# Kernel tuning notes

Hardware: AMD Instinct MI355X
Metric: run time of the kernel (lower is better)

## Reference

```python
import jax, jax.numpy as jnp
import numpy as np

B, L, DIM, N, D = 8, 273, 1536, 12, 128
ZS, F_HIS = 256, 32  # image tokens per frame, cache_frame_max
EPS = 1e-6


def rmsnorm(x, g, eps=EPS):
    return x * jax.lax.rsqrt(jnp.mean(x * x, axis=-1, keepdims=True) + eps) * g


def rope_apply(x, freqs):
    # x: [B, T, N, D]; freqs: [T, D//2] angles. Rotate consecutive pairs.
    xp = x.reshape(*x.shape[:-1], D // 2, 2)
    c = jnp.cos(freqs)[None, :, None, :]
    s = jnp.sin(freqs)[None, :, None, :]
    o1 = xp[..., 0] * c - xp[..., 1] * s
    o2 = xp[..., 0] * s + xp[..., 1] * c
    return jnp.stack([o1, o2], axis=-1).reshape(x.shape)


def setup_inputs() -> dict:
    key = jax.random.key(0)
    ks = jax.random.split(key, 10)
    rn = lambda k, shp, sc=1.0: jax.random.normal(k, shp, dtype=jnp.float32) * sc
    return {
        "x": rn(ks[0], (B, L, DIM)),
        "w_q": rn(ks[1], (DIM, DIM), 0.02), "b_q": jnp.zeros((DIM,), jnp.float32),
        "w_k": rn(ks[2], (DIM, DIM), 0.02), "b_k": jnp.zeros((DIM,), jnp.float32),
        "w_v": rn(ks[3], (DIM, DIM), 0.02), "b_v": jnp.zeros((DIM,), jnp.float32),
        "w_o": rn(ks[4], (DIM, DIM), 0.02), "b_o": jnp.zeros((DIM,), jnp.float32),
        "g_q": jnp.ones((DIM,), jnp.float32), "g_k": jnp.ones((DIM,), jnp.float32),
        "cache_k": rn(ks[5], (B, F_HIS * L, N, D)),
        "cache_v": rn(ks[6], (B, F_HIS * L, N, D)),
        "rope_table": jax.random.uniform(ks[7], (64, L, D // 2), dtype=jnp.float32) * (2.0 * np.pi),
        "read_rope_indices": jnp.arange(F_HIS, dtype=jnp.int32),
        "current_frame_idx": 20,
    }


def reference(x, w_q, b_q, w_k, b_k, w_v, b_v, w_o, b_o, g_q, g_k,
              cache_k, cache_v, rope_table, read_rope_indices, current_frame_idx):
    b, s = x.shape[:2]
    f = 1  # one new frame per step (s == L)
    # qkv projections with RMSNorm over full dim (pre head split)
    q = rmsnorm(x @ w_q.T + b_q, g_q).reshape(b, s, N, D)
    k = rmsnorm(x @ w_k.T + b_k, g_k).reshape(b, s, N, D)
    v = (x @ w_v.T + b_v).reshape(b, s, N, D)
    # KV-cache ring-buffer store at slot = frame_idx % cache_frame_max
    slot = current_frame_idx % F_HIS
    cache_k = jax.lax.dynamic_update_slice(cache_k, k, (0, slot * L, 0, 0))
    cache_v = jax.lax.dynamic_update_slice(cache_v, v, (0, slot * L, 0, 0))
    # RoPE angles: history for each cache slot, last for the current frame
    freqs_his = rope_table[read_rope_indices].reshape(F_HIS * L, D // 2)
    freqs_last = rope_table[current_frame_idx]  # [L, D//2]
    q_r = rope_apply(q, freqs_last)
    k_r = rope_apply(cache_k, freqs_his)
    # frame-major views: [b, frames, tokens_per_frame, n, d]
    q_r = q_r.reshape(b, f, L, N, D)
    k_r = k_r.reshape(b, F_HIS, L, N, D)
    v_his = cache_v.reshape(b, F_HIS, L, N, D)
    q_img, k_img, v_img = q_r[:, :, :ZS], k_r[:, :, :ZS], v_his[:, :, :ZS]
    # temporal attention per spatial (image) token, non-causal, masked to valid frames
    scale = 1.0 / jnp.sqrt(jnp.asarray(D, jnp.float32))
    scores = jnp.einsum('bfznd,bgznd->bznfg', q_img, k_img) * scale  # [b,zs,n,f,f_his]
    valid = jnp.minimum(current_frame_idx + 1, F_HIS)
    keep = jnp.arange(F_HIS) < valid
    scores = jnp.where(keep[None, None, None, None, :], scores, -1e30)
    p = jax.nn.softmax(scores, axis=-1)
    x_img = jnp.einsum('bznfg,bgznd->bfznd', p, v_img)  # [b, f, zs, n, d]
    # condition tokens bypass attention: pass through v of the current frame
    v_cond = v.reshape(b, f, L, N, D)[:, :, ZS:]
    out = jnp.concatenate([x_img, v_cond], axis=2).reshape(b, s, N * D)
    return out @ w_o.T + b_o


if __name__ == '__main__':
    o = reference(**setup_inputs())
    print(o.shape)
```

## Files before the change

kernel.cpp:

```cpp
#include <hip/hip_runtime.h>
#include <hip/hip_bf16.h>
#include <stdint.h>

typedef unsigned short u16;
typedef __attribute__((ext_vector_type(8))) short bf16x8;
typedef __attribute__((ext_vector_type(4))) float f32x4;

#define B_    8
#define L_    273
#define DIM_  1536
#define NH_   12
#define DH_   128
#define ZS_   256
#define FH_   32
#define MROWS (B_ * L_)
#define MPAD  2304
#define NQKV  4608

#define OFF_XB    0ULL
#define OFF_WB    7077888ULL
#define OFF_WOB   21233664ULL
#define OFF_BQKV  25952256ULL
#define OFF_CQKV  25970688ULL
#define OFF_ATTN  47204352ULL
#define OFF_SC    54282240ULL

__device__ __forceinline__ u16 f2bf(float f) {
  __hip_bfloat16 h = __float2bfloat16(f);
  return *reinterpret_cast<u16*>(&h);
}
__device__ __forceinline__ float bf2f(u16 v) {
  uint32_t u = ((uint32_t)v) << 16;
  return __uint_as_float(u);
}

__device__ __forceinline__ void gload_lds16(const u16* g, u16* l) {
  __builtin_amdgcn_global_load_lds(
      (const __attribute__((address_space(1))) void*)g,
      (__attribute__((address_space(3))) void*)l,
      16, 0, 0);
}

__global__ void cast_pad8_kernel(const float* __restrict__ src, u16* __restrict__ dst,
                                 int n_src8, int n_tot8) {
  int i = blockIdx.x * 256 + threadIdx.x;
  if (i >= n_tot8) return;
  uint4 o;
  if (i < n_src8) {
    const float4 a = ((const float4*)src)[i * 2];
    const float4 b = ((const float4*)src)[i * 2 + 1];
    o.x = (uint32_t)f2bf(a.x) | ((uint32_t)f2bf(a.y) << 16);
    o.y = (uint32_t)f2bf(a.z) | ((uint32_t)f2bf(a.w) << 16);
    o.z = (uint32_t)f2bf(b.x) | ((uint32_t)f2bf(b.y) << 16);
    o.w = (uint32_t)f2bf(b.z) | ((uint32_t)f2bf(b.w) << 16);
  } else {
    o = make_uint4(0, 0, 0, 0);
  }
  ((uint4*)dst)[i] = o;
}

__global__ void pack_bias_kernel(const float* __restrict__ bq, const float* __restrict__ bk,
                                 const float* __restrict__ bv, float* __restrict__ dst) {
  int i = blockIdx.x * 256 + threadIdx.x;
  if (i >= NQKV) return;
  float v;
  if (i < DIM_)            v = bq[i];
  else if (i < 2 * DIM_)   v = bk[i - DIM_];
  else                     v = bv[i - 2 * DIM_];
  dst[i] = v;
}

__global__ __launch_bounds__(256)
void sincos_kernel(const float* __restrict__ rope_table, const int* __restrict__ rope_idx,
                   float* __restrict__ sctab) {
  const int idx = blockIdx.x * 4 + (threadIdx.x >> 6);
  const int j = threadIdx.x & 63;
  const int f = idx / ZS_, z = idx % ZS_;
  const int fi = rope_idx[f];
  const float fr = rope_table[((size_t)fi * L_ + z) * 64 + j];
  float sn, cn;
  __sincosf(fr, &sn, &cn);
  *(float2*)&sctab[((size_t)idx << 7) + 2 * j] = make_float2(sn, cn);
}

__global__ __launch_bounds__(256)
void gemm_bt_kernel(const u16* __restrict__ A, const u16* __restrict__ Bm,
                    const float* __restrict__ bias, void* __restrict__ Cv,
                    int K, int ldc, int Mvalid, int bf16out) {
  const int tn = blockIdx.x, tm = blockIdx.y;
  const int tid = threadIdx.x;
  const int lane = tid & 63;
  const int wid = tid >> 6;
  const int wm = wid >> 1, wn = wid & 1;

  __shared__ __align__(16) u16 As[128 * 32];
  __shared__ __align__(16) u16 Bs[128 * 32];

  f32x4 acc[4][4] = {};

  const int srow = tid >> 2;
  const int scol = (tid & 3) * 8;
  const u16* Abase = A + (size_t)(tm * 128 + srow) * K + scol;
  const u16* Bbase = Bm + (size_t)(tn * 128 + srow) * K + scol;
  u16* lAs = &As[srow * 32 + scol];
  u16* lBs = &Bs[srow * 32 + scol];
  const size_t rstep = (size_t)64 * K;

  const int ko = (lane >> 4) * 8;
  const int rA = wm * 64 + (lane & 15);
  const int rB = wn * 64 + (lane & 15);

  for (int kt = 0; kt < K; kt += 32) {
    __syncthreads();
    gload_lds16(Abase + kt,         lAs);
    gload_lds16(Abase + kt + rstep, lAs + 64 * 32);
    gload_lds16(Bbase + kt,         lBs);
    gload_lds16(Bbase + kt + rstep, lBs + 64 * 32);
    __syncthreads();

    bf16x8 af[4], bfr[4];
#pragma unroll
    for (int f = 0; f < 4; ++f) {
      af[f]  = *(const bf16x8*)&As[(rA + f * 16) * 32 + ko];
      bfr[f] = *(const bf16x8*)&Bs[(rB + f * 16) * 32 + ko];
    }
#pragma unroll
    for (int fm = 0; fm < 4; ++fm)
#pragma unroll
      for (int fn = 0; fn < 4; ++fn)
        acc[fm][fn] = __builtin_amdgcn_mfma_f32_16x16x32_bf16(af[fm], bfr[fn], acc[fm][fn], 0, 0, 0);
  }

  const int m0 = tm * 128 + wm * 64 + (lane >> 4) * 4;
  const int n0 = tn * 128 + wn * 64 + (lane & 15);
#pragma unroll
  for (int fm = 0; fm < 4; ++fm) {
#pragma unroll
    for (int fn = 0; fn < 4; ++fn) {
      const int n = n0 + fn * 16;
      const float bv = bias[n];
#pragma unroll
      for (int r = 0; r < 4; ++r) {
        const int m = m0 + fm * 16 + r;
        if (m < Mvalid) {
          const float val = acc[fm][fn][r] + bv;
          if (bf16out) ((u16*)Cv)[(size_t)m * ldc + n] = f2bf(val);
          else         ((float*)Cv)[(size_t)m * ldc + n] = val;
        }
      }
    }
  }
}

__global__ __launch_bounds__(256)
void rmsnorm_rope_kernel(u16* __restrict__ C, const float* __restrict__ g_q,
                         const float* __restrict__ g_k, const float* __restrict__ rope_table,
                         const int* __restrict__ cf_ptr) {
  const int z = blockIdx.x % ZS_;
  const int b = blockIdx.x / ZS_;
  const int m = b * L_ + z;
  const int tid = threadIdx.x;
  const int cf = *cf_ptr;
  u16* row = C + (size_t)m * NQKV;
  __shared__ float red[4];

  for (int sec = 0; sec < 2; ++sec) {
    u16* p = row + sec * DIM_;
    const float* gw = sec ? g_k : g_q;
    float vx[3], vy[3];
    float ss = 0.f;
#pragma unroll
    for (int j = 0; j < 3; ++j) {
      int pj = tid + j * 256;
      uint32_t u = *(const uint32_t*)&p[pj * 2];
      vx[j] = bf2f((u16)(u & 0xffff));
      vy[j] = bf2f((u16)(u >> 16));
      ss += vx[j] * vx[j] + vy[j] * vy[j];
    }
#pragma unroll
    for (int o = 32; o; o >>= 1) ss += __shfl_xor(ss, o);
    if ((tid & 63) == 0) red[tid >> 6] = ss;
    __syncthreads();
    const float tot = red[0] + red[1] + red[2] + red[3];
    const float r = rsqrtf(tot * (1.f / DIM_) + 1e-6f);
#pragma unroll
    for (int j = 0; j < 3; ++j) {
      int pj = tid + j * 256;
      float y0 = vx[j] * r * gw[pj * 2];
      float y1 = vy[j] * r * gw[pj * 2 + 1];
      if (sec == 0) {
        float fr = rope_table[((size_t)cf * L_ + z) * 64 + (pj & 63)];
        float sn, cn;
        __sincosf(fr, &sn, &cn);
        float o0 = y0 * cn - y1 * sn;
        float o1 = y0 * sn + y1 * cn;
        y0 = o0; y1 = o1;
      }
      *(uint32_t*)&p[pj * 2] = (uint32_t)f2bf(y0) | ((uint32_t)f2bf(y1) << 16);
    }
    __syncthreads();
  }
}

__global__ __launch_bounds__(256)
void attention_kernel(const u16* __restrict__ Cq, const float* __restrict__ cache_k,
                      const float* __restrict__ cache_v, const float* __restrict__ sctab,
                      const int* __restrict__ cf_ptr, u16* __restrict__ attn_in) {
  const int w = blockIdx.x * 4 + (threadIdx.x >> 6);
  const int lane = threadIdx.x & 63;
  const int hp = w % 6;
  const int z = (w / 6) % ZS_;
  const int b = w / (6 * ZS_);
  const int h = lane >> 5, il = lane & 31;
  const int n = hp * 2 + h;
  const int d0 = il * 4;
  const int cf = *cf_ptr;
  const int slot = cf % FH_;
  const int valid = min(cf + 1, FH_);

  const size_t crow = (size_t)(b * L_ + z) * NQKV + n * DH_ + d0;
  float q0, q1, q2, q3;
  {
    ushort4 qv = *(const ushort4*)&Cq[crow];
    q0 = bf2f(qv.x); q1 = bf2f(qv.y); q2 = bf2f(qv.z); q3 = bf2f(qv.w);
  }

  float mx = -1e30f, lsum = 0.f;
  float a0 = 0.f, a1 = 0.f, a2 = 0.f, a3 = 0.f;
  for (int g = 0; g < valid; ++g) {
    const float4 sc = *(const float4*)&sctab[((size_t)(g * ZS_ + z) << 7) + d0];
    float k0, k1, k2, k3, v0, v1, v2, v3;
    if (g == slot) {
      ushort4 kv = *(const ushort4*)&Cq[crow + DIM_];
      ushort4 vv = *(const ushort4*)&Cq[crow + 2 * DIM_];
      k0 = bf2f(kv.x); k1 = bf2f(kv.y); k2 = bf2f(kv.z); k3 = bf2f(kv.w);
      v0 = bf2f(vv.x); v1 = bf2f(vv.y); v2 = bf2f(vv.z); v3 = bf2f(vv.w);
    } else {
      const size_t coff = ((((size_t)b * FH_ + g) * L_ + z) * NH_ + n) * DH_ + d0;
      const float4 kk = *(const float4*)&cache_k[coff];
      const float4 vv = *(const float4*)&cache_v[coff];
      k0 = kk.x; k1 = kk.y; k2 = kk.z; k3 = kk.w;
      v0 = vv.x; v1 = vv.y; v2 = vv.z; v3 = vv.w;
    }
    const float kr0 = k0 * sc.y - k1 * sc.x;
    const float kr1 = k0 * sc.x + k1 * sc.y;
    const float kr2 = k2 * sc.w - k3 * sc.z;
    const float kr3 = k2 * sc.z + k3 * sc.w;
    float part = q0 * kr0 + q1 * kr1 + q2 * kr2 + q3 * kr3;
#pragma unroll
    for (int o = 16; o; o >>= 1) part += __shfl_xor(part, o);
    const float score = part * 0.088388347648318447f;
    const float nm = fmaxf(mx, score);
    const float scl = __expf(mx - nm);
    const float pw = __expf(score - nm);
    lsum = lsum * scl + pw;
    a0 = a0 * scl + pw * v0;
    a1 = a1 * scl + pw * v1;
    a2 = a2 * scl + pw * v2;
    a3 = a3 * scl + pw * v3;
    mx = nm;
  }
  const float inv = 1.f / lsum;
  uint2 o;
  o.x = (uint32_t)f2bf(a0 * inv) | ((uint32_t)f2bf(a1 * inv) << 16);
  o.y = (uint32_t)f2bf(a2 * inv) | ((uint32_t)f2bf(a3 * inv) << 16);
  *(uint2*)&attn_in[(size_t)(b * L_ + z) * DIM_ + n * DH_ + d0] = o;
}

__global__ void vcond_kernel(const u16* __restrict__ Cq, u16* __restrict__ attn_in) {
  int i = blockIdx.x * 256 + threadIdx.x;
  const int tot = B_ * (L_ - ZS_) * DIM_ / 8;
  if (i >= tot) return;
  int e = i * 8;
  int col = e % DIM_;
  int r = e / DIM_;
  int b = r / (L_ - ZS_);
  int lz = r % (L_ - ZS_);
  size_t mrow = (size_t)b * L_ + ZS_ + lz;
  *(uint4*)&attn_in[mrow * DIM_ + col] = *(const uint4*)&Cq[mrow * NQKV + 2 * DIM_ + col];
}

extern "C" void kernel_launch(void* const* d_in, const int* in_sizes, int n_in,
                              void* d_out, int out_size, void* d_ws, size_t ws_size,
                              hipStream_t stream) {
  const float* x       = (const float*)d_in[0];
  const float* w_q     = (const float*)d_in[1];
  const float* b_q     = (const float*)d_in[2];
  const float* w_k     = (const float*)d_in[3];
  const float* b_k     = (const float*)d_in[4];
  const float* w_v     = (const float*)d_in[5];
  const float* b_v     = (const float*)d_in[6];
  const float* w_o     = (const float*)d_in[7];
  const float* b_o     = (const float*)d_in[8];
  const float* g_q     = (const float*)d_in[9];
  const float* g_k     = (const float*)d_in[10];
  const float* cache_k = (const float*)d_in[11];
  const float* cache_v = (const float*)d_in[12];
  const float* rope_tb = (const float*)d_in[13];
  const int*   rope_ix = (const int*)d_in[14];
  const int*   cf      = (const int*)d_in[15];

  char* ws = (char*)d_ws;
  u16*   xb      = (u16*)(ws + OFF_XB);
  u16*   wb      = (u16*)(ws + OFF_WB);
  u16*   wob     = (u16*)(ws + OFF_WOB);
  float* bqkv    = (float*)(ws + OFF_BQKV);
  u16*   Cq      = (u16*)(ws + OFF_CQKV);
  u16*   attn_in = (u16*)(ws + OFF_ATTN);
  float* sctab   = (float*)(ws + OFF_SC);

  const int WN = DIM_ * DIM_;
  const int WN8 = WN / 8;
  const int X8 = MROWS * DIM_ / 8;
  const int XT8 = MPAD * DIM_ / 8;

  cast_pad8_kernel<<<(XT8 + 255) / 256, 256, 0, stream>>>(x, xb, X8, XT8);
  cast_pad8_kernel<<<(WN8 + 255) / 256, 256, 0, stream>>>(w_q, wb,          WN8, WN8);
  cast_pad8_kernel<<<(WN8 + 255) / 256, 256, 0, stream>>>(w_k, wb + WN,     WN8, WN8);
  cast_pad8_kernel<<<(WN8 + 255) / 256, 256, 0, stream>>>(w_v, wb + 2 * WN, WN8, WN8);
  cast_pad8_kernel<<<(WN8 + 255) / 256, 256, 0, stream>>>(w_o, wob,         WN8, WN8);
  pack_bias_kernel<<<(NQKV + 255) / 256, 256, 0, stream>>>(b_q, b_k, b_v, bqkv);
  sincos_kernel<<<FH_ * ZS_ / 4, 256, 0, stream>>>(rope_tb, rope_ix, sctab);

  gemm_bt_kernel<<<dim3(NQKV / 128, MPAD / 128), 256, 0, stream>>>(xb, wb, bqkv, Cq, DIM_, NQKV, MPAD, 1);

  rmsnorm_rope_kernel<<<B_ * ZS_, 256, 0, stream>>>(Cq, g_q, g_k, rope_tb, cf);

  attention_kernel<<<(B_ * ZS_ * 6) / 4, 256, 0, stream>>>(Cq, cache_k, cache_v, sctab, cf, attn_in);

  vcond_kernel<<<(B_ * (L_ - ZS_) * DIM_ / 8 + 255) / 256, 256, 0, stream>>>(Cq, attn_in);

  gemm_bt_kernel<<<dim3(DIM_ / 128, MPAD / 128), 256, 0, stream>>>(attn_in, wob, b_o, (float*)d_out, DIM_, DIM_, MROWS, 0);
}
```

Baseline: 250.1 us.

## Fuse prep kernels, double-buffer GEMM, split-K output projection, split attention frames

Merges the five casts, bias packing and sincos table into one prep kernel, and folds the v_cond copy into the attention launch to cut launch count. The GEMM gains double-buffered LDS so global loads overlap MFMA work. The output projection is split-K into two partial buffers (reusing workspace regions) with a separate reduce kernel adding bias. Attention splits each item's frame loop across two waves and merges them with an online-softmax combine through LDS. Split-K adds extra fp32 traffic and a reduce pass, and the partial buffers overlap earlier workspace regions.

```diff
diff --git a/kernel.cpp b/kernel.cpp
--- a/kernel.cpp
+++ b/kernel.cpp
@@ -16,6 +16,26 @@
 #define MROWS (B_ * L_)
 #define MPAD  2304
 #define NQKV  4608
+#define WN_   (DIM_ * DIM_)
+#define WN8_  (WN_ / 8)
+#define X8_   (MROWS * DIM_ / 8)
+#define XT8_  (MPAD * DIM_ / 8)
+
+#define N0_ 442368
+#define N1_ 737280
+#define N2_ 1032192
+#define N3_ 1327104
+#define N4_ 1622016
+#define N5_ 1626624
+#define N6_ 2150912
+#define PREP_BLKS 8402
+
+#define ATTN_ITEMS (B_ * ZS_ * 6)
+#define ATTN_BLKS  (ATTN_ITEMS / 2)
+#define VCOND_TOT  (B_ * (L_ - ZS_) * DIM_ / 8)
+#define VCOND_BLKS ((VCOND_TOT + 255) / 256)
+
+#define KSPLIT 768
 
 #define OFF_XB    0ULL
 #define OFF_WB    7077888ULL
@@ -24,6 +44,8 @@
 #define OFF_CQKV  25970688ULL
 #define OFF_ATTN  47204352ULL
 #define OFF_SC    54282240ULL
+#define OFF_P0    0ULL
+#define OFF_P1    25970688ULL
 
 __device__ __forceinline__ u16 f2bf(float f) {
   __hip_bfloat16 h = __float2bfloat16(f);
@@ -41,14 +63,12 @@
       16, 0, 0);
 }
 
-__global__ void cast_pad8_kernel(const float* __restrict__ src, u16* __restrict__ dst,
-                                 int n_src8, int n_tot8) {
-  int i = blockIdx.x * 256 + threadIdx.x;
-  if (i >= n_tot8) return;
+__device__ __forceinline__ void cast8(const float* __restrict__ s, u16* __restrict__ d,
+                                      int i, int nvalid) {
   uint4 o;
-  if (i < n_src8) {
-    const float4 a = ((const float4*)src)[i * 2];
-    const float4 b = ((const float4*)src)[i * 2 + 1];
+  if (i < nvalid) {
+    const float4 a = ((const float4*)s)[i * 2];
+    const float4 b = ((const float4*)s)[i * 2 + 1];
     o.x = (uint32_t)f2bf(a.x) | ((uint32_t)f2bf(a.y) << 16);
     o.y = (uint32_t)f2bf(a.z) | ((uint32_t)f2bf(a.w) << 16);
     o.z = (uint32_t)f2bf(b.x) | ((uint32_t)f2bf(b.y) << 16);
@@ -56,45 +76,56 @@
   } else {
     o = make_uint4(0, 0, 0, 0);
   }
-  ((uint4*)dst)[i] = o;
-}
-
-__global__ void pack_bias_kernel(const float* __restrict__ bq, const float* __restrict__ bk,
-                                 const float* __restrict__ bv, float* __restrict__ dst) {
-  int i = blockIdx.x * 256 + threadIdx.x;
-  if (i >= NQKV) return;
-  float v;
-  if (i < DIM_)            v = bq[i];
-  else if (i < 2 * DIM_)   v = bk[i - DIM_];
-  else                     v = bv[i - 2 * DIM_];
-  dst[i] = v;
+  ((uint4*)d)[i] = o;
 }
 
 __global__ __launch_bounds__(256)
-void sincos_kernel(const float* __restrict__ rope_table, const int* __restrict__ rope_idx,
-                   float* __restrict__ sctab) {
-  const int idx = blockIdx.x * 4 + (threadIdx.x >> 6);
-  const int j = threadIdx.x & 63;
-  const int f = idx / ZS_, z = idx % ZS_;
-  const int fi = rope_idx[f];
-  const float fr = rope_table[((size_t)fi * L_ + z) * 64 + j];
-  float sn, cn;
-  __sincosf(fr, &sn, &cn);
-  *(float2*)&sctab[((size_t)idx << 7) + 2 * j] = make_float2(sn, cn);
+void prep_kernel(const float* __restrict__ x, const float* __restrict__ w_q,
+                 const float* __restrict__ w_k, const float* __restrict__ w_v,
+                 const float* __restrict__ w_o, const float* __restrict__ bq,
+                 const float* __restrict__ bk, const float* __restrict__ bv,
+                 const float* __restrict__ rope_tb, const int* __restrict__ rope_ix,
+                 u16* __restrict__ xb, u16* __restrict__ wb, u16* __restrict__ wob,
+                 float* __restrict__ bqkv, float* __restrict__ sctab) {
+  const int t = blockIdx.x * 256 + threadIdx.x;
+  if (t < N0_)      cast8(x,   xb,           t,       X8_);
+  else if (t < N1_) cast8(w_q, wb,           t - N0_, WN8_);
+  else if (t < N2_) cast8(w_k, wb + WN_,     t - N1_, WN8_);
+  else if (t < N3_) cast8(w_v, wb + 2 * WN_, t - N2_, WN8_);
+  else if (t < N4_) cast8(w_o, wob,          t - N3_, WN8_);
+  else if (t < N5_) {
+    int i = t - N4_;
+    float v;
+    if (i < DIM_)          v = bq[i];
+    else if (i < 2 * DIM_) v = bk[i - DIM_];
+    else                   v = bv[i - 2 * DIM_];
+    bqkv[i] = v;
+  } else {
+    int u = t - N5_;
+    int j = u & 63;
+    int idx = u >> 6;
+    int f = idx >> 8, z = idx & 255;
+    int fi = rope_ix[f];
+    float fr = rope_tb[((size_t)fi * L_ + z) * 64 + j];
+    float sn, cn;
+    __sincosf(fr, &sn, &cn);
+    *(float2*)&sctab[((size_t)idx << 7) + 2 * j] = make_float2(sn, cn);
+  }
 }
 
 __global__ __launch_bounds__(256)
 void gemm_bt_kernel(const u16* __restrict__ A, const u16* __restrict__ Bm,
                     const float* __restrict__ bias, void* __restrict__ Cv,
-                    int K, int ldc, int Mvalid, int bf16out) {
+                    void* __restrict__ Cv2,
+                    int K, int ldc, int Mvalid, int mode, int ksplit) {
   const int tn = blockIdx.x, tm = blockIdx.y;
   const int tid = threadIdx.x;
   const int lane = tid & 63;
   const int wid = tid >> 6;
   const int wm = wid >> 1, wn = wid & 1;
 
-  __shared__ __align__(16) u16 As[128 * 32];
-  __shared__ __align__(16) u16 Bs[128 * 32];
+  __shared__ __align__(16) u16 As[2][128 * 32];
+  __shared__ __align__(16) u16 Bs[2][128 * 32];
 
   f32x4 acc[4][4] = {};
 
@@ -102,50 +133,62 @@
   const int scol = (tid & 3) * 8;
   const u16* Abase = A + (size_t)(tm * 128 + srow) * K + scol;
   const u16* Bbase = Bm + (size_t)(tn * 128 + srow) * K + scol;
-  u16* lAs = &As[srow * 32 + scol];
-  u16* lBs = &Bs[srow * 32 + scol];
   const size_t rstep = (size_t)64 * K;
+  const int lofs = srow * 32 + scol;
 
   const int ko = (lane >> 4) * 8;
   const int rA = wm * 64 + (lane & 15);
   const int rB = wn * 64 + (lane & 15);
 
-  for (int kt = 0; kt < K; kt += 32) {
-    __syncthreads();
-    gload_lds16(Abase + kt,         lAs);
-    gload_lds16(Abase + kt + rstep, lAs + 64 * 32);
-    gload_lds16(Bbase + kt,         lBs);
-    gload_lds16(Bbase + kt + rstep, lBs + 64 * 32);
-    __syncthreads();
-
+  const int k0 = blockIdx.z * ksplit;
+  const int k1 = k0 + ksplit;
+
+  gload_lds16(Abase + k0,         &As[0][lofs]);
+  gload_lds16(Abase + k0 + rstep, &As[0][64 * 32 + lofs]);
+  gload_lds16(Bbase + k0,         &Bs[0][lofs]);
+  gload_lds16(Bbase + k0 + rstep, &Bs[0][64 * 32 + lofs]);
+  __syncthreads();
+
+  int cur = 0;
+  for (int kt = k0; kt < k1; kt += 32) {
+    const int nx = cur ^ 1;
+    if (kt + 32 < k1) {
+      gload_lds16(Abase + kt + 32,         &As[nx][lofs]);
+      gload_lds16(Abase + kt + 32 + rstep, &As[nx][64 * 32 + lofs]);
+      gload_lds16(Bbase + kt + 32,         &Bs[nx][lofs]);
+      gload_lds16(Bbase + kt + 32 + rstep, &Bs[nx][64 * 32 + lofs]);
+    }
     bf16x8 af[4], bfr[4];
 #pragma unroll
     for (int f = 0; f < 4; ++f) {
-      af[f]  = *(const bf16x8*)&As[(rA + f * 16) * 32 + ko];
-      bfr[f] = *(const bf16x8*)&Bs[(rB + f * 16) * 32 + ko];
+      af[f]  = *(const bf16x8*)&As[cur][(rA + f * 16) * 32 + ko];
+      bfr[f] = *(const bf16x8*)&Bs[cur][(rB + f * 16) * 32 + ko];
     }
 #pragma unroll
     for (int fm = 0; fm < 4; ++fm)
 #pragma unroll
       for (int fn = 0; fn < 4; ++fn)
         acc[fm][fn] = __builtin_amdgcn_mfma_f32_16x16x32_bf16(af[fm], bfr[fn], acc[fm][fn], 0, 0, 0);
+    __syncthreads();
+    cur = nx;
   }
 
   const int m0 = tm * 128 + wm * 64 + (lane >> 4) * 4;
   const int n0 = tn * 128 + wn * 64 + (lane & 15);
+  float* Cf = (mode == 2 && blockIdx.z) ? (float*)Cv2 : (float*)Cv;
 #pragma unroll
   for (int fm = 0; fm < 4; ++fm) {
 #pragma unroll
     for (int fn = 0; fn < 4; ++fn) {
       const int n = n0 + fn * 16;
-      const float bv = bias[n];
+      const float bv = (mode == 2) ? 0.f : bias[n];
 #pragma unroll
       for (int r = 0; r < 4; ++r) {
         const int m = m0 + fm * 16 + r;
         if (m < Mvalid) {
           const float val = acc[fm][fn][r] + bv;
-          if (bf16out) ((u16*)Cv)[(size_t)m * ldc + n] = f2bf(val);
-          else         ((float*)Cv)[(size_t)m * ldc + n] = val;
+          if (mode == 1) ((u16*)Cv)[(size_t)m * ldc + n] = f2bf(val);
+          else           Cf[(size_t)m * ldc + n] = val;
         }
       }
     }
@@ -206,17 +249,37 @@
 void attention_kernel(const u16* __restrict__ Cq, const float* __restrict__ cache_k,
                       const float* __restrict__ cache_v, const float* __restrict__ sctab,
                       const int* __restrict__ cf_ptr, u16* __restrict__ attn_in) {
-  const int w = blockIdx.x * 4 + (threadIdx.x >> 6);
+  if (blockIdx.x >= ATTN_BLKS) {
+    int i = (blockIdx.x - ATTN_BLKS) * 256 + threadIdx.x;
+    if (i < VCOND_TOT) {
+      int e = i * 8;
+      int col = e % DIM_;
+      int r = e / DIM_;
+      int b = r / (L_ - ZS_);
+      int lz = r % (L_ - ZS_);
+      size_t mrow = (size_t)b * L_ + ZS_ + lz;
+      *(uint4*)&attn_in[mrow * DIM_ + col] = *(const uint4*)&Cq[mrow * NQKV + 2 * DIM_ + col];
+    }
+    return;
+  }
+
+  __shared__ float sm[2][64][6];
+  const int p = threadIdx.x >> 7;
+  const int wi = (threadIdx.x >> 6) & 1;
   const int lane = threadIdx.x & 63;
-  const int hp = w % 6;
-  const int z = (w / 6) % ZS_;
-  const int b = w / (6 * ZS_);
+  const int item = blockIdx.x * 2 + p;
+  const int hp = item % 6;
+  const int z = (item / 6) % ZS_;
+  const int b = item / (6 * ZS_);
   const int h = lane >> 5, il = lane & 31;
   const int n = hp * 2 + h;
   const int d0 = il * 4;
   const int cf = *cf_ptr;
   const int slot = cf % FH_;
   const int valid = min(cf + 1, FH_);
+  const int g0 = (valid + 1) >> 1;
+  const int gs = wi ? g0 : 0;
+  const int ge = wi ? valid : g0;
 
   const size_t crow = (size_t)(b * L_ + z) * NQKV + n * DH_ + d0;
   float q0, q1, q2, q3;
@@ -227,7 +290,7 @@
 
   float mx = -1e30f, lsum = 0.f;
   float a0 = 0.f, a1 = 0.f, a2 = 0.f, a3 = 0.f;
-  for (int g = 0; g < valid; ++g) {
+  for (int g = gs; g < ge; ++g) {
     const float4 sc = *(const float4*)&sctab[((size_t)(g * ZS_ + z) << 7) + d0];
     float k0, k1, k2, k3, v0, v1, v2, v3;
     if (g == slot) {
@@ -260,24 +323,45 @@
     a3 = a3 * scl + pw * v3;
     mx = nm;
   }
-  const float inv = 1.f / lsum;
-  uint2 o;
-  o.x = (uint32_t)f2bf(a0 * inv) | ((uint32_t)f2bf(a1 * inv) << 16);
-  o.y = (uint32_t)f2bf(a2 * inv) | ((uint32_t)f2bf(a3 * inv) << 16);
-  *(uint2*)&attn_in[(size_t)(b * L_ + z) * DIM_ + n * DH_ + d0] = o;
-}
-
-__global__ void vcond_kernel(const u16* __restrict__ Cq, u16* __restrict__ attn_in) {
-  int i = blockIdx.x * 256 + threadIdx.x;
-  const int tot = B_ * (L_ - ZS_) * DIM_ / 8;
-  if (i >= tot) return;
-  int e = i * 8;
-  int col = e % DIM_;
-  int r = e / DIM_;
-  int b = r / (L_ - ZS_);
-  int lz = r % (L_ - ZS_);
-  size_t mrow = (size_t)b * L_ + ZS_ + lz;
-  *(uint4*)&attn_in[mrow * DIM_ + col] = *(const uint4*)&Cq[mrow * NQKV + 2 * DIM_ + col];
+
+  if (wi == 1) {
+    sm[p][lane][0] = mx;  sm[p][lane][1] = lsum;
+    sm[p][lane][2] = a0;  sm[p][lane][3] = a1;
+    sm[p][lane][4] = a2;  sm[p][lane][5] = a3;
+  }
+  __syncthreads();
+  if (wi == 0) {
+    const float mB = sm[p][lane][0], lB = sm[p][lane][1];
+    const float M = fmaxf(mx, mB);
+    const float wA = __expf(mx - M), wB = __expf(mB - M);
+    const float L = lsum * wA + lB * wB;
+    const float inv = 1.f / L;
+    const float o0 = (a0 * wA + sm[p][lane][2] * wB) * inv;
+    const float o1 = (a1 * wA + sm[p][lane][3] * wB) * inv;
+    const float o2 = (a2 * wA + sm[p][lane][4] * wB) * inv;
+    const float o3 = (a3 * wA + sm[p][lane][5] * wB) * inv;
+    uint2 o;
+    o.x = (uint32_t)f2bf(o0) | ((uint32_t)f2bf(o1) << 16);
+    o.y = (uint32_t)f2bf(o2) | ((uint32_t)f2bf(o3) << 16);
+    *(uint2*)&attn_in[(size_t)(b * L_ + z) * DIM_ + n * DH_ + d0] = o;
+  }
+}
+
+__global__ __launch_bounds__(256)
+void reduce_kernel(const float* __restrict__ p0, const float* __restrict__ p1,
+                   const float* __restrict__ b_o, float* __restrict__ out) {
+  const int i = blockIdx.x * 256 + threadIdx.x;
+  if (i >= MROWS * DIM_ / 4) return;
+  const int col4 = i % (DIM_ / 4);
+  const float4 a = ((const float4*)p0)[i];
+  const float4 b = ((const float4*)p1)[i];
+  const float4 c = ((const float4*)b_o)[col4];
+  float4 o;
+  o.x = a.x + b.x + c.x;
+  o.y = a.y + b.y + c.y;
+  o.z = a.z + b.z + c.z;
+  o.w = a.w + b.w + c.w;
+  ((float4*)out)[i] = o;
 }
 
 extern "C" void kernel_launch(void* const* d_in, const int* in_sizes, int n_in,
@@ -308,27 +392,22 @@
   u16*   Cq      = (u16*)(ws + OFF_CQKV);
   u16*   attn_in = (u16*)(ws + OFF_ATTN);
   float* sctab   = (float*)(ws + OFF_SC);
-
-  const int WN = DIM_ * DIM_;
-  const int WN8 = WN / 8;
-  const int X8 = MROWS * DIM_ / 8;
-  const int XT8 = MPAD * DIM_ / 8;
-
-  cast_pad8_kernel<<<(XT8 + 255) / 256, 256, 0, stream>>>(x, xb, X8, XT8);
-  cast_pad8_kernel<<<(WN8 + 255) / 256, 256, 0, stream>>>(w_q, wb,          WN8, WN8);
-  cast_pad8_kernel<<<(WN8 + 255) / 256, 256, 0, stream>>>(w_k, wb + WN,     WN8, WN8);
-  cast_pad8_kernel<<<(WN8 + 255) / 256, 256, 0, stream>>>(w_v, wb + 2 * WN, WN8, WN8);
-  cast_pad8_kernel<<<(WN8 + 255) / 256, 256, 0, stream>>>(w_o, wob,         WN8, WN8);
-  pack_bias_kernel<<<(NQKV + 255) / 256, 256, 0, stream>>>(b_q, b_k, b_v, bqkv);
-  sincos_kernel<<<FH_ * ZS_ / 4, 256, 0, stream>>>(rope_tb, rope_ix, sctab);
-
-  gemm_bt_kernel<<<dim3(NQKV / 128, MPAD / 128), 256, 0, stream>>>(xb, wb, bqkv, Cq, DIM_, NQKV, MPAD, 1);
+  float* p0      = (float*)(ws + OFF_P0);
+  float* p1      = (float*)(ws + OFF_P1);
+
+  prep_kernel<<<PREP_BLKS, 256, 0, stream>>>(x, w_q, w_k, w_v, w_o, b_q, b_k, b_v,
+                                             rope_tb, rope_ix, xb, wb, wob, bqkv, sctab);
+
+  gemm_bt_kernel<<<dim3(NQKV / 128, MPAD / 128, 1), 256, 0, stream>>>(
+      xb, wb, bqkv, Cq, nullptr, DIM_, NQKV, MPAD, 1, DIM_);
 
   rmsnorm_rope_kernel<<<B_ * ZS_, 256, 0, stream>>>(Cq, g_q, g_k, rope_tb, cf);
 
-  attention_kernel<<<(B_ * ZS_ * 6) / 4, 256, 0, stream>>>(Cq, cache_k, cache_v, sctab, cf, attn_in);
-
-  vcond_kernel<<<(B_ * (L_ - ZS_) * DIM_ / 8 + 255) / 256, 256, 0, stream>>>(Cq, attn_in);
-
-  gemm_bt_kernel<<<dim3(DIM_ / 128, MPAD / 128), 256, 0, stream>>>(attn_in, wob, b_o, (float*)d_out, DIM_, DIM_, MROWS, 0);
-}
+  attention_kernel<<<ATTN_BLKS + VCOND_BLKS, 256, 0, stream>>>(
+      Cq, cache_k, cache_v, sctab, cf, attn_in);
+
+  gemm_bt_kernel<<<dim3(DIM_ / 128, MPAD / 128, 2), 256, 0, stream>>>(
+      attn_in, wob, nullptr, p0, p1, DIM_, DIM_, MPAD, 2, KSPLIT);
+
+  reduce_kernel<<<(MROWS * DIM_ / 4 + 255) / 256, 256, 0, stream>>>(p0, p1, b_o, (float*)d_out);
+}
```

Result: faster. 224.0 us (-10.4%).
